# Optimization experiments

Measured on AMD Instinct MI355X. Metric: run time of the kernel, lower is better.

The kernel has to match this reference:

```python
import jax, jax.numpy as jnp
import numpy as np

NUM_HEADS = 16
HEAD_DIM = 128
D = NUM_HEADS * HEAD_DIM  # 2048
B, S = 4, 2048
NEG = jnp.finfo(jnp.float32).min


def setup_inputs() -> dict:
    key = jax.random.key(0)
    ks = jax.random.split(key, 6)
    scale = 1.0 / np.sqrt(D)
    return {
        "hidden_states": jax.random.normal(ks[0], (B, S, D), jnp.float32),
        "wq": jax.random.normal(ks[1], (D, D), jnp.float32) * scale,
        "wk": jax.random.normal(ks[2], (D, D), jnp.float32) * scale,
        "wv": jax.random.normal(ks[3], (D, D), jnp.float32) * scale,
        "wo": jax.random.normal(ks[4], (D, D), jnp.float32) * scale,
        "bo": jnp.zeros((D,), jnp.float32),
    }


def _split_heads(x):
    b, s, _ = x.shape
    return x.reshape(b, s, NUM_HEADS, HEAD_DIM).transpose(0, 2, 1, 3)  # [B,H,S,Dh]


def reference(hidden_states, wq, wk, wv, wo, bo):
    # projections (nn.Linear: x @ W^T), no bias for q/k/v
    q = _split_heads(hidden_states @ wq.T).astype(jnp.float32)
    k = _split_heads(hidden_states @ wk.T).astype(jnp.float32)
    v = _split_heads(hidden_states @ wv.T)
    # GPT-Neo: NO 1/sqrt(d) scaling
    scores = jnp.einsum("bhqd,bhkd->bhqk", q, k)  # [B,H,S,S] fp32
    s = scores.shape[-1]
    causal = jnp.tril(jnp.ones((s, s), bool))  # [S,S]
    scores = jnp.where(causal[None, None], scores, NEG)
    attn_weights = jax.nn.softmax(scores, axis=-1).astype(v.dtype)
    # dropout is identity at eval (p=0.0)
    attn_output = jnp.einsum("bhqk,bhkd->bhqd", attn_weights, v)
    attn_output = attn_output.transpose(0, 2, 1, 3).reshape(hidden_states.shape)
    attn_output = attn_output @ wo.T + bo
    return attn_output, attn_weights
```

## Files before the change

kernel.cpp:

```cpp
#include <hip/hip_runtime.h>

#define DEVFN static __device__ __forceinline__

typedef _Float16 f16;
typedef f16 f16x8 __attribute__((ext_vector_type(8)));
typedef f16 f16x4 __attribute__((ext_vector_type(4)));
typedef float f32x4 __attribute__((ext_vector_type(4)));
typedef short short8 __attribute__((ext_vector_type(8)));

constexpr int Bc = 4, Hn = 16, Sn = 2048, DH = 128, Dn = 2048;
constexpr long MROWS = (long)Bc * Sn;
constexpr long LDQK = 2 * Dn;

template <typename T, typename C>
DEVFN auto mfma_impl(T a, T b, C c, int)
    -> decltype(__builtin_amdgcn_mfma_f32_16x16x32_f16(a, b, c, 0, 0, 0)) {
  return __builtin_amdgcn_mfma_f32_16x16x32_f16(a, b, c, 0, 0, 0);
}
template <typename T, typename C>
DEVFN C mfma_impl(T a, T b, C c, long) {
  return __builtin_amdgcn_mfma_f32_16x16x32_f16(
      __builtin_bit_cast(short8, a), __builtin_bit_cast(short8, b), c, 0, 0, 0);
}
DEVFN f32x4 MFMA(f16x8 a, f16x8 b, f32x4 c) { return mfma_impl(a, b, c, 0); }

DEVFN void nt_store(float* p, float v) { __builtin_nontemporal_store(v, p); }
DEVFN void nt_store4(float* p, f32x4 v) {
  __builtin_nontemporal_store(v, (f32x4*)p);
}

DEVFN void gld_lds16(const f16* g, f16* s) {
  __builtin_amdgcn_global_load_lds(
      (const __attribute__((address_space(1))) unsigned int*)g,
      (__attribute__((address_space(3))) unsigned int*)s, 16, 0, 0);
}

DEVFN void stage_tile(const f16* __restrict__ g, long ld, f16* __restrict__ s) {
  const int t = threadIdx.x;
  const int rr = t >> 3;
  const int cb = (t & 7) * 16;
#pragma unroll
  for (int ch = 0; ch < 4; ++ch) {
    const int r = ch * 32 + rr;
    const int scb = cb ^ ((r & 7) << 4);
    gld_lds16(g + (long)r * ld + (scb >> 1), s + r * 64 + (cb >> 1));
  }
}

DEVFN void stage_tile128(const f16* __restrict__ g, long ld, f16* __restrict__ s) {
  const int t = threadIdx.x;
  const int rr = t >> 4;
  const int cb = (t & 15) * 16;
#pragma unroll
  for (int ch = 0; ch < 8; ++ch) {
    const int r = ch * 16 + rr;
    const int scb = cb ^ ((r & 7) << 4);
    gld_lds16(g + (long)r * ld + (scb >> 1), s + r * 128 + (cb >> 1));
  }
}

DEVFN f16x8 ldfrag(const f16* s, int row, int kelem) {
  const int cb = (kelem * 2) ^ ((row & 7) << 4);
  return *(const f16x8*)(s + row * 64 + (cb >> 1));
}

DEVFN f16x8 ldfrag128(const f16* s, int row, int kelem) {
  const int cb = (kelem * 2) ^ ((row & 7) << 4);
  return *(const f16x8*)((const char*)s + row * 256 + cb);
}

DEVFN f16x8 ldfrag64(const f16* s, int row, int kelem) {
  const int cb = (kelem * 2) ^ ((row & 7) << 4);
  return *(const f16x8*)((const char*)s + row * 128 + cb);
}

__global__ __launch_bounds__(256) void k_cvt_all(
    const float* __restrict__ hid, const float* __restrict__ wq,
    const float* __restrict__ wk, const float* __restrict__ wv,
    const float* __restrict__ wo, f16* __restrict__ h16,
    f16* __restrict__ wqk16, f16* __restrict__ wv16, f16* __restrict__ wo16) {
  const int y = blockIdx.y;
  const long nW = (long)Dn * Dn;
  const float* x;
  f16* out;
  if (y < 4) {
    x = hid + (long)y * nW;
    out = h16 + (long)y * nW;
  } else if (y == 4) {
    x = wq; out = wqk16;
  } else if (y == 5) {
    x = wk; out = wqk16 + nW;
  } else if (y == 6) {
    x = wv; out = wv16;
  } else {
    x = wo; out = wo16;
  }
  const long i = ((long)blockIdx.x * 256 + threadIdx.x) * 4;
  float4 v = *(const float4*)(x + i);
  f16x4 h;
  h[0] = (f16)v.x; h[1] = (f16)v.y; h[2] = (f16)v.z; h[3] = (f16)v.w;
  *(f16x4*)(out + i) = h;
}

DEVFN void gemm_body(const f16* __restrict__ A, long ldA,
                     const f16* __restrict__ B, long ldB, int K,
                     f16* __restrict__ oh, long ldC, int nt, int mt,
                     f16* sA, f16* sB) {
  const int tid = threadIdx.x, w = tid >> 6, lane = tid & 63;
  const int wm = (w >> 1) * 64, wn = (w & 1) * 64;
  const int lr = lane & 15, lg = lane >> 4;
  f32x4 acc[4][4] = {};
  const f16* Ab = A + (long)mt * 128 * ldA;
  const f16* Bb = B + (long)nt * 128 * ldB;

  stage_tile(Ab, ldA, sA);
  stage_tile(Bb, ldB, sB);
  __syncthreads();

  int cur = 0;
  for (int kt = 0; kt < K; kt += 64) {
    if (kt + 64 < K) {
      stage_tile(Ab + kt + 64, ldA, sA + (cur ^ 1) * (128 * 64));
      stage_tile(Bb + kt + 64, ldB, sB + (cur ^ 1) * (128 * 64));
    }
    const f16* cA = sA + cur * (128 * 64);
    const f16* cB = sB + cur * (128 * 64);
#pragma unroll
    for (int kk = 0; kk < 64; kk += 32) {
      f16x8 ahf[4], bhf[4];
#pragma unroll
      for (int m = 0; m < 4; ++m) ahf[m] = ldfrag(cA, wm + m * 16 + lr, kk + lg * 8);
#pragma unroll
      for (int n = 0; n < 4; ++n) bhf[n] = ldfrag(cB, wn + n * 16 + lr, kk + lg * 8);
#pragma unroll
      for (int m = 0; m < 4; ++m)
#pragma unroll
        for (int n = 0; n < 4; ++n) acc[m][n] = MFMA(ahf[m], bhf[n], acc[m][n]);
    }
    __syncthreads();
    cur ^= 1;
  }

#pragma unroll
  for (int m = 0; m < 4; ++m)
#pragma unroll
    for (int n = 0; n < 4; ++n) {
      const int col = nt * 128 + wn + n * 16 + lr;
#pragma unroll
      for (int r = 0; r < 4; ++r) {
        const long row = (long)mt * 128 + wm + m * 16 + lg * 4 + r;
        oh[row * ldC + col] = (f16)acc[m][n][r];
      }
    }
}

__global__ __launch_bounds__(256) void k_fused(
    const f16* __restrict__ h16, const f16* __restrict__ wqk16,
    const f16* __restrict__ wv16, f16* __restrict__ qk16, f16* __restrict__ vT,
    float* __restrict__ wts) {
  __shared__ __align__(16) f16 sA[2 * 128 * 64];
  __shared__ __align__(16) f16 sB[2 * 128 * 64];
  const int bid = blockIdx.x;
  if ((bid & 3) == 3) {
    const int zid = bid >> 2;
    const int bh = zid & 63, qt = zid >> 6;
    const int ncols = Sn - (qt + 1) * 128;
    if (ncols <= 0) return;
    float* base = wts + (long)bh * Sn * Sn + (long)qt * 128 * Sn + (qt + 1) * 128;
    const int tid = threadIdx.x;
    const f32x4 z = {0.f, 0.f, 0.f, 0.f};
    for (int r = 0; r < 128; ++r) {
      float* rowp = base + (long)r * Sn;
      for (int c = tid * 4; c < ncols; c += 1024) nt_store4(rowp + c, z);
    }
    return;
  }
  const int gid = 3 * (bid >> 2) + (bid & 3);
  if (gid < 2048) {
    const int cpx = 2048 >> 3;
    const int swz = (gid & 7) * cpx + (gid >> 3);
    const int nt = swz & 31, mt = swz >> 5;
    gemm_body(h16, Dn, wqk16, Dn, Dn, qk16, LDQK, nt, mt, sA, sB);
  } else {
    const int sb = gid - 2048;
    const int cpx = 1024 >> 3;
    const int swz = (sb & 7) * cpx + (sb >> 3);
    const int nt = swz & 63, mt = swz >> 6;
    gemm_body(wv16, Dn, h16, Dn, Dn, vT, MROWS, nt, mt, sA, sB);
  }
}

__global__ __launch_bounds__(256) void k_gemm_wo(
    const f16* __restrict__ A, const f16* __restrict__ B,
    float* __restrict__ of, const float* __restrict__ bias) {
  const int nwgx = gridDim.x;
  const int nwg = nwgx * gridDim.y;
  const int bid = blockIdx.y * nwgx + blockIdx.x;
  const int cpx = nwg >> 3;
  const int swz = (bid & 7) * cpx + (bid >> 3);
  const int nt = swz % nwgx, mt = swz / nwgx;
  __shared__ __align__(16) f16 sA[2][128 * 64];
  __shared__ __align__(16) f16 sB[2][128 * 64];
  const int tid = threadIdx.x, w = tid >> 6, lane = tid & 63;
  const int wm = (w >> 1) * 64, wn = (w & 1) * 64;
  const int lr = lane & 15, lg = lane >> 4;
  f32x4 acc[4][4] = {};
  const f16* Ab = A + (long)mt * 128 * Dn;
  const f16* Bb = B + (long)nt * 128 * Dn;

  stage_tile(Ab, Dn, sA[0]);
  stage_tile(Bb, Dn, sB[0]);
  __syncthreads();

  int cur = 0;
  for (int kt = 0; kt < Dn; kt += 64) {
    if (kt + 64 < Dn) {
      stage_tile(Ab + kt + 64, Dn, sA[cur ^ 1]);
      stage_tile(Bb + kt + 64, Dn, sB[cur ^ 1]);
    }
#pragma unroll
    for (int kk = 0; kk < 64; kk += 32) {
      f16x8 ahf[4], bhf[4];
#pragma unroll
      for (int m = 0; m < 4; ++m) ahf[m] = ldfrag(sA[cur], wm + m * 16 + lr, kk + lg * 8);
#pragma unroll
      for (int n = 0; n < 4; ++n) bhf[n] = ldfrag(sB[cur], wn + n * 16 + lr, kk + lg * 8);
#pragma unroll
      for (int m = 0; m < 4; ++m)
#pragma unroll
        for (int n = 0; n < 4; ++n) acc[m][n] = MFMA(ahf[m], bhf[n], acc[m][n]);
    }
    __syncthreads();
    cur ^= 1;
  }

#pragma unroll
  for (int m = 0; m < 4; ++m)
#pragma unroll
    for (int n = 0; n < 4; ++n) {
      const int col = nt * 128 + wn + n * 16 + lr;
#pragma unroll
      for (int r = 0; r < 4; ++r) {
        const long row = (long)mt * 128 + wm + m * 16 + lg * 4 + r;
        nt_store(of + row * Dn + col, acc[m][n][r] + bias[col]);
      }
    }
}

__global__ __launch_bounds__(256) void k_attn(const f16* __restrict__ qk16,
                                              const f16* __restrict__ vT,
                                              float* __restrict__ wts,
                                              f16* __restrict__ ctx) {
  const int wgid = blockIdx.x;
  const int xcd = wgid & 7, slot = wgid >> 3;
  const int bh = xcd + 8 * (slot >> 4);
  const int qt = 15 - (slot & 15);
  const int b = bh >> 4, h = bh & 15;
  const int tid = threadIdx.x, wv = tid >> 6, lane = tid & 63;
  const int lr = lane & 15, lg = lane >> 4;
  const f16* Qb = qk16 + ((long)b * Sn + qt * 128) * LDQK + h * DH;
  const f16* Kb = qk16 + (long)b * Sn * LDQK + Dn + h * DH;
  const f16* Vb = vT + (long)h * DH * MROWS + (long)b * Sn;
  float* Wrow = wts + (long)bh * Sn * Sn + (long)qt * 128 * Sn;
  __shared__ __align__(16) f16 sK[2][128 * 128];
  __shared__ __align__(16) f16 sQW[128 * 64];

  const int krr = tid >> 4;
  const int kce = (tid & 15) * 8;
  const int kcb = kce * 2;
  f16x8 kpf[8];

#define PRE_K(kt_)                                                              \
  {                                                                             \
    const long kbase = (long)(kt_)*128;                                         \
    _Pragma("unroll") for (int ch = 0; ch < 8; ++ch) kpf[ch] =                  \
        *(const f16x8*)(Kb + (kbase + ch * 16 + krr) * LDQK + kce);             \
  }
#define PUB_K(buf)                                                              \
  {                                                                             \
    _Pragma("unroll") for (int ch = 0; ch < 8; ++ch) {                          \
      const int r = ch * 16 + krr;                                              \
      *(f16x8*)((char*)(buf) + r * 256 + (kcb ^ ((r & 7) << 4))) = kpf[ch];     \
    }                                                                           \
  }

  stage_tile128(Qb, LDQK, sK[0]);
  PRE_K(0);
  __syncthreads();
  const int wq0 = wv * 32;
  f16x8 qf[2][4];
#pragma unroll
  for (int m = 0; m < 2; ++m)
#pragma unroll
    for (int kk = 0; kk < 4; ++kk)
      qf[m][kk] = ldfrag128(sK[0], wq0 + m * 16 + lr, kk * 32 + lg * 8);
  __syncthreads();
  PUB_K(sK[0]);
  if (qt > 0) PRE_K(1);
  __syncthreads();
  int cur = 0;

  float rs[2][4] = {};
  for (int kt = 0; kt <= qt; ++kt) {
    f32x4 acc[2][8] = {};
#pragma unroll
    for (int kk = 0; kk < 4; ++kk) {
      f16x8 bf[8];
#pragma unroll
      for (int n = 0; n < 8; ++n) bf[n] = ldfrag128(sK[cur], n * 16 + lr, kk * 32 + lg * 8);
#pragma unroll
      for (int m = 0; m < 2; ++m)
#pragma unroll
        for (int n = 0; n < 8; ++n) acc[m][n] = MFMA(qf[m][kk], bf[n], acc[m][n]);
    }
    if (kt + 1 <= qt) PUB_K(sK[cur ^ 1]);
    PRE_K(kt + 2 <= qt ? kt + 2 : 0);
    const bool diag = (kt == qt);
#pragma unroll
    for (int m = 0; m < 2; ++m)
#pragma unroll
      for (int r = 0; r < 4; ++r) {
        const int row = wq0 + m * 16 + lg * 4 + r;
        float ts = 0.f;
#pragma unroll
        for (int n = 0; n < 8; ++n) {
          const bool ok = !diag || (n * 16 + lr) <= row;
          ts += ok ? __expf(acc[m][n][r]) : 0.f;
        }
#pragma unroll
        for (int o = 1; o < 16; o <<= 1) ts += __shfl_xor(ts, o, 64);
        rs[m][r] += ts;
      }
    __syncthreads();
    cur ^= 1;
  }
  float ri[2][4];
#pragma unroll
  for (int m = 0; m < 2; ++m)
#pragma unroll
    for (int r = 0; r < 4; ++r) ri[m][r] = 1.f / rs[m][r];

  PUB_K(sK[cur ^ 1]);
  if (qt > 0) PRE_K(1);
  __syncthreads();
  cur ^= 1;

  f32x4 pacc[2][8] = {};
  for (int kt = 0; kt <= qt; ++kt) {
    f32x4 sacc[2][8] = {};
#pragma unroll
    for (int kk = 0; kk < 4; ++kk) {
      f16x8 bf[8];
#pragma unroll
      for (int n = 0; n < 8; ++n) bf[n] = ldfrag128(sK[cur], n * 16 + lr, kk * 32 + lg * 8);
#pragma unroll
      for (int m = 0; m < 2; ++m)
#pragma unroll
        for (int n = 0; n < 8; ++n) sacc[m][n] = MFMA(qf[m][kk], bf[n], sacc[m][n]);
    }
    if (kt + 1 <= qt) PUB_K(sK[cur ^ 1]);
    if (kt + 2 <= qt) PRE_K(kt + 2);
    const bool diag = (kt == qt);
#pragma unroll
    for (int hf = 0; hf < 2; ++hf) {
#pragma unroll
      for (int m = 0; m < 2; ++m)
#pragma unroll
        for (int n = hf * 4; n < hf * 4 + 4; ++n) {
          const int col = n * 16 + lr;
          const int scol = col - hf * 64;
#pragma unroll
          for (int r = 0; r < 4; ++r) {
            const int row = wq0 + m * 16 + lg * 4 + r;
            float w = __expf(sacc[m][n][r]) * ri[m][r];
            if (diag && col > row) w = 0.f;
            nt_store(Wrow + (long)row * Sn + kt * 128 + col, w);
            *(f16*)((char*)sQW + row * 128 + ((scol * 2) ^ ((row & 7) << 4))) = (f16)w;
          }
        }
#pragma unroll
      for (int kk = 0; kk < 2; ++kk) {
        f16x8 af[2], bfr[8];
#pragma unroll
        for (int m = 0; m < 2; ++m)
          af[m] = ldfrag64(sQW, wq0 + m * 16 + lr, kk * 32 + lg * 8);
#pragma unroll
        for (int n = 0; n < 8; ++n)
          bfr[n] = *(const f16x8*)(Vb + (long)(n * 16 + lr) * MROWS + kt * 128 + hf * 64 + kk * 32 + lg * 8);
#pragma unroll
        for (int m = 0; m < 2; ++m)
#pragma unroll
          for (int n = 0; n < 8; ++n) pacc[m][n] = MFMA(af[m], bfr[n], pacc[m][n]);
      }
    }
    __syncthreads();
    cur ^= 1;
  }

#pragma unroll
  for (int m = 0; m < 2; ++m)
#pragma unroll
    for (int n = 0; n < 8; ++n) {
      const int d = n * 16 + lr;
#pragma unroll
      for (int r = 0; r < 4; ++r) {
        const int q = qt * 128 + wq0 + m * 16 + lg * 4 + r;
        ctx[(long)(b * Sn + q) * Dn + h * DH + d] = (f16)pacc[m][n][r];
      }
    }
#undef PRE_K
#undef PUB_K
}

extern "C" void kernel_launch(void* const* d_in, const int* in_sizes, int n_in,
                              void* d_out, int out_size, void* d_ws, size_t ws_size,
                              hipStream_t stream) {
  const float* hid = (const float*)d_in[0];
  const float* wq = (const float*)d_in[1];
  const float* wk = (const float*)d_in[2];
  const float* wv = (const float*)d_in[3];
  const float* wo = (const float*)d_in[4];
  const float* bo = (const float*)d_in[5];
  float* out = (float*)d_out;
  float* wts = out + (long)Bc * Sn * Dn;

  char* ws = (char*)d_ws;
  const long MB = 1 << 20;
  f16* h16 = (f16*)(ws + 0 * MB);
  f16* wqk16 = (f16*)(ws + 32 * MB);
  f16* wv16 = (f16*)(ws + 48 * MB);
  f16* wo16 = (f16*)(ws + 56 * MB);
  f16* qk16 = (f16*)(ws + 64 * MB);
  f16* vT = (f16*)(ws + 128 * MB);
  f16* ctx = (f16*)(ws + 160 * MB);

  k_cvt_all<<<dim3(4096, 8), 256, 0, stream>>>(
      hid, wq, wk, wv, wo, h16, wqk16, wv16, wo16);
  k_fused<<<4096, 256, 0, stream>>>(h16, wqk16, wv16, qk16, vT, wts);
  k_attn<<<1024, 256, 0, stream>>>(qk16, vT, wts, ctx);
  k_gemm_wo<<<dim3(16, 64), 256, 0, stream>>>(ctx, wo16, out, bo);
}
```

Baseline: 815.9 us.

## Vectorize attention-weight stores via LDS readback and use exp2 with prescaled Q

The fp32 attention-weight matrix was written with scattered 4-byte non-temporal stores straight from MFMA fragments. It is now read back from the swizzled f16 LDS tile that already feeds the PV MFMA and written as contiguous 16-byte stores. Separately, the Q columns are scaled by log2(e) in the projection epilogue so the softmax can use the hardware exp2 instruction. The per-tile row-sum shuffle reduction is also moved out of the K loop and done once. The risk is precision: stored weights are now rounded to f16 before widening back to fp32, and the extra LDS reads add traffic.

Measured after the change: 805.8 us. Within noise of the previous version (-1.2%).

```diff
diff --git a/kernel.cpp b/kernel.cpp
--- a/kernel.cpp
+++ b/kernel.cpp
@@ -105,7 +105,7 @@
 DEVFN void gemm_body(const f16* __restrict__ A, long ldA,
                      const f16* __restrict__ B, long ldB, int K,
                      f16* __restrict__ oh, long ldC, int nt, int mt,
-                     f16* sA, f16* sB) {
+                     float oscale, f16* sA, f16* sB) {
   const int tid = threadIdx.x, w = tid >> 6, lane = tid & 63;
   const int wm = (w >> 1) * 64, wn = (w & 1) * 64;
   const int lr = lane & 15, lg = lane >> 4;
@@ -149,7 +149,7 @@
 #pragma unroll
       for (int r = 0; r < 4; ++r) {
         const long row = (long)mt * 128 + wm + m * 16 + lg * 4 + r;
-        oh[row * ldC + col] = (f16)acc[m][n][r];
+        oh[row * ldC + col] = (f16)(acc[m][n][r] * oscale);
       }
     }
 }
@@ -180,13 +180,14 @@
     const int cpx = 2048 >> 3;
     const int swz = (gid & 7) * cpx + (gid >> 3);
     const int nt = swz & 31, mt = swz >> 5;
-    gemm_body(h16, Dn, wqk16, Dn, Dn, qk16, LDQK, nt, mt, sA, sB);
+    const float qsc = (nt < 16) ? 1.44269504f : 1.0f;
+    gemm_body(h16, Dn, wqk16, Dn, Dn, qk16, LDQK, nt, mt, qsc, sA, sB);
   } else {
     const int sb = gid - 2048;
     const int cpx = 1024 >> 3;
     const int swz = (sb & 7) * cpx + (sb >> 3);
     const int nt = swz & 63, mt = swz >> 6;
-    gemm_body(wv16, Dn, h16, Dn, Dn, vT, MROWS, nt, mt, sA, sB);
+    gemm_body(wv16, Dn, h16, Dn, Dn, vT, MROWS, nt, mt, 1.0f, sA, sB);
   }
 }
 
@@ -325,10 +326,8 @@
 #pragma unroll
         for (int n = 0; n < 8; ++n) {
           const bool ok = !diag || (n * 16 + lr) <= row;
-          ts += ok ? __expf(acc[m][n][r]) : 0.f;
+          ts += ok ? __builtin_amdgcn_exp2f(acc[m][n][r]) : 0.f;
         }
-#pragma unroll
-        for (int o = 1; o < 16; o <<= 1) ts += __shfl_xor(ts, o, 64);
         rs[m][r] += ts;
       }
     __syncthreads();
@@ -338,13 +337,19 @@
 #pragma unroll
   for (int m = 0; m < 2; ++m)
 #pragma unroll
-    for (int r = 0; r < 4; ++r) ri[m][r] = 1.f / rs[m][r];
+    for (int r = 0; r < 4; ++r) {
+      float s = rs[m][r];
+#pragma unroll
+      for (int o = 1; o < 16; o <<= 1) s += __shfl_xor(s, o, 64);
+      ri[m][r] = 1.f / s;
+    }
 
   PUB_K(sK[cur ^ 1]);
   if (qt > 0) PRE_K(1);
   __syncthreads();
   cur ^= 1;
 
+  const int ro = lane >> 3, cg = lane & 7;
   f32x4 pacc[2][8] = {};
   for (int kt = 0; kt <= qt; ++kt) {
     f32x4 sacc[2][8] = {};
@@ -372,12 +377,21 @@
 #pragma unroll
           for (int r = 0; r < 4; ++r) {
             const int row = wq0 + m * 16 + lg * 4 + r;
-            float w = __expf(sacc[m][n][r]) * ri[m][r];
+            float w = __builtin_amdgcn_exp2f(sacc[m][n][r]) * ri[m][r];
             if (diag && col > row) w = 0.f;
-            nt_store(Wrow + (long)row * Sn + kt * 128 + col, w);
             *(f16*)((char*)sQW + row * 128 + ((scol * 2) ^ ((row & 7) << 4))) = (f16)w;
           }
         }
+#pragma unroll
+      for (int it = 0; it < 4; ++it) {
+        const int row = wq0 + it * 8 + ro;
+        f16x8 v = ldfrag64(sQW, row, cg * 8);
+        f32x4 lo = {(float)v[0], (float)v[1], (float)v[2], (float)v[3]};
+        f32x4 hi = {(float)v[4], (float)v[5], (float)v[6], (float)v[7]};
+        float* wp = Wrow + (long)row * Sn + kt * 128 + hf * 64 + cg * 8;
+        nt_store4(wp, lo);
+        nt_store4(wp + 4, hi);
+      }
 #pragma unroll
       for (int kk = 0; kk < 2; ++kk) {
         f16x8 af[2], bfr[8];
```
